# Optimization experiments

Hardware: AMD Instinct MI355X
Metric: run time of the kernel (lower is better)

The kernel has to match this reference:

```python
import jax, jax.numpy as jnp
import numpy as np

B, S, D = 32, 4096, 512

def setup_inputs() -> dict:
    key = jax.random.key(0)
    ks = jax.random.split(key, 5)
    scale = 1.0 / np.sqrt(D)
    return {
        "query": jax.random.normal(ks[0], (B, D), jnp.float32),
        "values": jax.random.normal(ks[1], (B, S, D), jnp.float32),
        "W1": jax.random.normal(ks[2], (D, D), jnp.float32) * scale,
        "b1": jnp.zeros((D,), jnp.float32),
        "W2": jax.random.normal(ks[3], (D, D), jnp.float32) * scale,
        "b2": jnp.zeros((D,), jnp.float32),
        "V": jax.random.normal(ks[4], (D, 1), jnp.float32) * scale,
        "bv": jnp.zeros((1,), jnp.float32),
    }

def reference(query, values, W1, b1, W2, b2, V, bv):
    # query: [B, D], values: [B, S, D]
    q_proj = query @ W1 + b1                      # [B, D]
    v_proj = jnp.einsum('bsd,de->bse', values, W2) + b2  # [B, S, D]
    hidden = jnp.tanh(q_proj[:, None, :] + v_proj)       # [B, S, D]
    score = jnp.einsum('bsd,de->bse', hidden, V) + bv    # [B, S, 1]
    attn = jax.nn.softmax(score, axis=1)                 # softmax over seq axis
    context = jnp.sum(attn * values, axis=1)             # [B, D]
    return (context, attn)
```

## Files before the change

kernel.cpp:

```cpp
#include <hip/hip_runtime.h>
#include <hip/hip_bf16.h>
#include <stdint.h>

#define NB 32
#define NS 4096
#define ND 512

typedef __attribute__((ext_vector_type(8))) short short8;
typedef __attribute__((ext_vector_type(4))) float floatx4;
typedef __attribute__((ext_vector_type(4))) unsigned int uint4v;

__device__ __forceinline__ short f2bf(float f) {
    unsigned int u = __builtin_bit_cast(unsigned int, f);
    return (short)((u + 0x8000u) >> 16);
}

__device__ __forceinline__ unsigned int cvt_pk_bf16(float lo, float hi) {
    unsigned int r;
    asm("v_cvt_pk_bf16_f32 %0, %1, %2" : "=v"(r) : "v"(lo), "v"(hi));
    return r;
}

__device__ __forceinline__ float fast_tanh(float x) {
    float e = __expf(2.0f * x);
    return 1.0f - 2.0f * __builtin_amdgcn_rcpf(e + 1.0f);
}

__global__ void __launch_bounds__(256) qproj_kernel(
    const float* __restrict__ query, const float* __restrict__ W1,
    const float* __restrict__ b1, const float* __restrict__ b2,
    float* __restrict__ qb) {
    const int b  = blockIdx.x;
    const int es = blockIdx.y;
    const int t  = threadIdx.x;
    const int col = t & 63, kc = t >> 6;
    __shared__ float q[ND];
    __shared__ float red[256];
    q[t] = query[b * ND + t];
    q[t + 256] = query[b * ND + t + 256];
    __syncthreads();
    float acc = 0.f;
    const float* wp = W1 + (size_t)(kc * 128) * ND + es * 64 + col;
    const float* qp = q + kc * 128;
#pragma unroll 8
    for (int k = 0; k < 128; k++)
        acc += qp[k] * wp[(size_t)k * ND];
    red[t] = acc;
    __syncthreads();
    if (t < 64) {
        float s = red[t] + red[t + 64] + red[t + 128] + red[t + 192];
        int e = es * 64 + t;
        qb[b * ND + e] = s + b1[e] + b2[e];
    }
}

__global__ void __launch_bounds__(256) w2t_kernel(
    const float* __restrict__ W2, unsigned short* __restrict__ W2Tt) {
    int g = blockIdx.x * 256 + threadIdx.x;
    int nt = g >> 14;
    int ks = (g >> 10) & 15;
    int kq = (g >> 8) & 3;
    int n  = g & 255;
    int e  = nt * 256 + n;
    int k0 = ks * 32 + kq * 8;
    short8 v;
#pragma unroll
    for (int j = 0; j < 8; j++)
        v[j] = f2bf(W2[(size_t)(k0 + j) * ND + e]);
    *(short8*)&W2Tt[(size_t)g * 8] = v;
}

__global__ void __launch_bounds__(256, 2) scores_kernel(
    const float* __restrict__ values, const unsigned short* __restrict__ W2Tt,
    const float* __restrict__ qb, const float* __restrict__ V,
    float* __restrict__ pscores) {
    const int st = blockIdx.x;
    const int b  = blockIdx.y;
    const int s0 = st * 64;

    __shared__ __align__(16) unsigned short sA[16][2048];
    __shared__ float sQb[ND];
    __shared__ float sV[ND];
    __shared__ float sRed[4][64];

    const int tid  = threadIdx.x;
    const int lane = tid & 63;
    const int wave = tid >> 6;
    const int mr = lane & 15;
    const int q  = lane >> 4;

    sQb[tid] = qb[b * ND + tid];
    sQb[tid + 256] = qb[b * ND + tid + 256];
    sV[tid]  = V[tid];
    sV[tid + 256] = V[tid + 256];

    const int arow = tid >> 2;
    const int ac   = tid & 3;
    const int ardo = arow * 32 + ((ac ^ ((tid >> 3) & 3)) * 8);
    const float* ag = values + ((size_t)b * NS + s0 + arow) * ND + ac * 8;

    {
        float4 aq[4][2];
#pragma unroll
        for (int u = 0; u < 4; u++) {
            aq[u][0] = *(const float4*)(ag + u * 32);
            aq[u][1] = *(const float4*)(ag + u * 32 + 4);
        }
#pragma unroll
        for (int ks = 0; ks < 16; ks++) {
            const float4 a0 = aq[ks & 3][0], a1 = aq[ks & 3][1];
            if (ks < 12) {
                aq[ks & 3][0] = *(const float4*)(ag + (ks + 4) * 32);
                aq[ks & 3][1] = *(const float4*)(ag + (ks + 4) * 32 + 4);
            }
            uint4v w;
            w.x = cvt_pk_bf16(a0.x, a0.y); w.y = cvt_pk_bf16(a0.z, a0.w);
            w.z = cvt_pk_bf16(a1.x, a1.y); w.w = cvt_pk_bf16(a1.z, a1.w);
            *(uint4v*)&sA[ks][ardo] = w;
        }
    }
    __syncthreads();

    const int afo = (q ^ ((mr >> 1) & 3)) * 8;
    const unsigned short* bp = W2Tt + (q * 256 + wave * 64 + mr) * 8;

    floatx4 acc[4][4] = {};
    float p[4][4] = {};
    short8 af[2][4], bq[2][4];

#pragma unroll
    for (int i = 0; i < 4; i++)
        af[0][i] = *(const short8*)&sA[0][(i * 16 + mr) * 32 + afo];
#pragma unroll
    for (int j = 0; j < 4; j++)
        bq[0][j] = *(const short8*)(bp + j * 128);

#pragma unroll
    for (int hk = 0; hk < 32; hk++) {
        const int cur = hk & 1, nxt = cur ^ 1;
        const int ks = hk & 15;

        if (hk < 31) {
            const unsigned short* bsrc = bp + (size_t)(hk + 1) * 8192;
#pragma unroll
            for (int j = 0; j < 4; j++)
                bq[nxt][j] = *(const short8*)(bsrc + j * 128);
#pragma unroll
            for (int i = 0; i < 4; i++)
                af[nxt][i] = *(const short8*)&sA[(hk + 1) & 15][(i * 16 + mr) * 32 + afo];
        }

        __builtin_amdgcn_s_setprio(1);
#pragma unroll
        for (int i = 0; i < 4; i++)
#pragma unroll
            for (int j = 0; j < 4; j++)
                acc[i][j] = __builtin_amdgcn_mfma_f32_16x16x32_bf16(af[cur][i], bq[cur][j], acc[i][j], 0, 0, 0);
        __builtin_amdgcn_s_setprio(0);

        if (ks == 15) {
            const int h = hk >> 4;
            float vcoef[4], qadd[4];
#pragma unroll
            for (int j = 0; j < 4; j++) {
                int col = h * 256 + wave * 64 + j * 16 + mr;
                vcoef[j] = sV[col];
                qadd[j]  = sQb[col];
            }
#pragma unroll
            for (int i = 0; i < 4; i++)
#pragma unroll
                for (int r = 0; r < 4; r++) {
                    float s = 0.f;
#pragma unroll
                    for (int j = 0; j < 4; j++)
                        s += fast_tanh(acc[i][j][r] + qadd[j]) * vcoef[j];
                    p[i][r] += s;
                    if (hk < 31) acc[i][0][r] = 0.f;
                }
            if (hk < 31) {
#pragma unroll
                for (int i = 0; i < 4; i++)
#pragma unroll
                    for (int j = 1; j < 4; j++)
                        acc[i][j] = floatx4{0.f, 0.f, 0.f, 0.f};
            }
        }
    }

#pragma unroll
    for (int i = 0; i < 4; i++) {
#pragma unroll
        for (int r = 0; r < 4; r++) {
            float v = p[i][r];
            v += __shfl_xor(v, 1);
            v += __shfl_xor(v, 2);
            v += __shfl_xor(v, 4);
            v += __shfl_xor(v, 8);
            if (mr == 0) sRed[wave][i * 16 + q * 4 + r] = v;
        }
    }
    __syncthreads();
    if (tid < 64) {
        float s = sRed[0][tid] + sRed[1][tid] + sRed[2][tid] + sRed[3][tid];
        pscores[(size_t)b * NS + s0 + tid] = s;
    }
}

__global__ void __launch_bounds__(256) softmax_kernel(
    const float* __restrict__ pscores, float* __restrict__ attn) {
    int b = blockIdx.x;
    int t = threadIdx.x;
    __shared__ float red[4];
    __shared__ float bcast[2];
    const float* sc = pscores + (size_t)b * NS;
    float v[16];
    float m = -1e30f;
#pragma unroll
    for (int i = 0; i < 16; i++) { v[i] = sc[t + i * 256]; m = fmaxf(m, v[i]); }
    for (int o = 32; o; o >>= 1) m = fmaxf(m, __shfl_xor(m, o));
    if ((t & 63) == 0) red[t >> 6] = m;
    __syncthreads();
    if (t == 0) bcast[0] = fmaxf(fmaxf(red[0], red[1]), fmaxf(red[2], red[3]));
    __syncthreads();
    m = bcast[0];
    float sum = 0.f;
#pragma unroll
    for (int i = 0; i < 16; i++) { v[i] = __expf(v[i] - m); sum += v[i]; }
    for (int o = 32; o; o >>= 1) sum += __shfl_xor(sum, o);
    if ((t & 63) == 0) red[t >> 6] = sum;
    __syncthreads();
    if (t == 0) bcast[1] = red[0] + red[1] + red[2] + red[3];
    __syncthreads();
    float inv = 1.0f / bcast[1];
    float* ao = attn + (size_t)b * NS;
#pragma unroll
    for (int i = 0; i < 16; i++) ao[t + i * 256] = v[i] * inv;
}

__global__ void __launch_bounds__(256) context_partial_kernel(
    const float* __restrict__ values, const float* __restrict__ attn,
    float* __restrict__ pctx) {
    int sc = blockIdx.x;
    int b  = blockIdx.y;
    int t  = threadIdx.x;
    __shared__ float sAttn[128];
    if (t < 128) sAttn[t] = attn[(size_t)b * NS + sc * 128 + t];
    __syncthreads();
    int d = t * 2;
    const float2* vp = (const float2*)(values + ((size_t)b * NS + sc * 128) * ND + d);
    float ax = 0.f, ay = 0.f;
#pragma unroll 8
    for (int s = 0; s < 128; s++) {
        float a = sAttn[s];
        float2 v = vp[(size_t)s * 256];
        ax += a * v.x; ay += a * v.y;
    }
    pctx[((size_t)sc * 32 + b) * ND + d]     = ax;
    pctx[((size_t)sc * 32 + b) * ND + d + 1] = ay;
}

__global__ void __launch_bounds__(256) context_reduce_kernel(
    const float* __restrict__ pctx, float* __restrict__ ctx) {
    int i = blockIdx.x * 256 + threadIdx.x;
    float s = 0.f;
#pragma unroll
    for (int p = 0; p < 32; p++) s += pctx[(size_t)p * (32 * ND) + i];
    ctx[i] = s;
}

extern "C" void kernel_launch(void* const* d_in, const int* in_sizes, int n_in,
                              void* d_out, int out_size, void* d_ws, size_t ws_size,
                              hipStream_t stream) {
    const float* query  = (const float*)d_in[0];
    const float* values = (const float*)d_in[1];
    const float* W1     = (const float*)d_in[2];
    const float* b1     = (const float*)d_in[3];
    const float* W2     = (const float*)d_in[4];
    const float* b2     = (const float*)d_in[5];
    const float* V      = (const float*)d_in[6];

    float* ctx_out  = (float*)d_out;
    float* attn_out = (float*)d_out + NB * ND;

    char* ws = (char*)d_ws;
    float*          qb      = (float*)ws;
    unsigned short* W2Tt    = (unsigned short*)(ws + (64 << 10));
    float*          pscores = (float*)(ws + (576 << 10));
    float*          pctx    = (float*)(ws + (1088 << 10));

    qproj_kernel<<<dim3(NB, 8), 256, 0, stream>>>(query, W1, b1, b2, qb);
    w2t_kernel<<<128, 256, 0, stream>>>(W2, W2Tt);
    scores_kernel<<<dim3(64, 32), 256, 0, stream>>>(values, W2Tt, qb, V, pscores);
    softmax_kernel<<<NB, 256, 0, stream>>>(pscores, attn_out);
    context_partial_kernel<<<dim3(32, 32), 256, 0, stream>>>(values, attn_out, pctx);
    context_reduce_kernel<<<64, 256, 0, stream>>>(pctx, ctx_out);
}
```

Baseline: 477.2 us.

## Fuse prep and softmax kernels, deepen B prefetch, use nontemporal value loads

Merges the q-projection and W2 transpose into one launch, and folds the softmax into the context-partial kernel so each block recomputes the row max and sum itself. The softmax_kernel launch and the attn read-back go away, at the cost of 32x redundant softmax reductions. In the scores kernel the W2 fragment prefetch is deepened to a 3-stage ring, which adds register pressure. The loads of values now use nontemporal hints to limit cache pollution.

New measurement: 459.9 us. 3.6% less time.

```diff
diff --git a/kernel.cpp b/kernel.cpp
--- a/kernel.cpp
+++ b/kernel.cpp
@@ -8,6 +8,7 @@
 
 typedef __attribute__((ext_vector_type(8))) short short8;
 typedef __attribute__((ext_vector_type(4))) float floatx4;
+typedef __attribute__((ext_vector_type(2))) float floatx2;
 typedef __attribute__((ext_vector_type(4))) unsigned int uint4v;
 
 __device__ __forceinline__ short f2bf(float f) {
@@ -26,48 +27,49 @@
     return 1.0f - 2.0f * __builtin_amdgcn_rcpf(e + 1.0f);
 }
 
-__global__ void __launch_bounds__(256) qproj_kernel(
+__global__ void __launch_bounds__(256) prep_kernel(
     const float* __restrict__ query, const float* __restrict__ W1,
     const float* __restrict__ b1, const float* __restrict__ b2,
-    float* __restrict__ qb) {
-    const int b  = blockIdx.x;
-    const int es = blockIdx.y;
+    const float* __restrict__ W2,
+    float* __restrict__ qb, unsigned short* __restrict__ W2Tt) {
+    const int bx = blockIdx.x;
     const int t  = threadIdx.x;
-    const int col = t & 63, kc = t >> 6;
-    __shared__ float q[ND];
-    __shared__ float red[256];
-    q[t] = query[b * ND + t];
-    q[t + 256] = query[b * ND + t + 256];
-    __syncthreads();
-    float acc = 0.f;
-    const float* wp = W1 + (size_t)(kc * 128) * ND + es * 64 + col;
-    const float* qp = q + kc * 128;
+    if (bx < 256) {
+        const int b  = bx >> 3;
+        const int es = bx & 7;
+        const int col = t & 63, kc = t >> 6;
+        __shared__ float q[ND];
+        __shared__ float red[256];
+        q[t] = query[b * ND + t];
+        q[t + 256] = query[b * ND + t + 256];
+        __syncthreads();
+        float acc = 0.f;
+        const float* wp = W1 + (size_t)(kc * 128) * ND + es * 64 + col;
+        const float* qp = q + kc * 128;
 #pragma unroll 8
-    for (int k = 0; k < 128; k++)
-        acc += qp[k] * wp[(size_t)k * ND];
-    red[t] = acc;
-    __syncthreads();
-    if (t < 64) {
-        float s = red[t] + red[t + 64] + red[t + 128] + red[t + 192];
-        int e = es * 64 + t;
-        qb[b * ND + e] = s + b1[e] + b2[e];
-    }
-}
-
-__global__ void __launch_bounds__(256) w2t_kernel(
-    const float* __restrict__ W2, unsigned short* __restrict__ W2Tt) {
-    int g = blockIdx.x * 256 + threadIdx.x;
-    int nt = g >> 14;
-    int ks = (g >> 10) & 15;
-    int kq = (g >> 8) & 3;
-    int n  = g & 255;
-    int e  = nt * 256 + n;
-    int k0 = ks * 32 + kq * 8;
-    short8 v;
-#pragma unroll
-    for (int j = 0; j < 8; j++)
-        v[j] = f2bf(W2[(size_t)(k0 + j) * ND + e]);
-    *(short8*)&W2Tt[(size_t)g * 8] = v;
+        for (int k = 0; k < 128; k++)
+            acc += qp[k] * wp[(size_t)k * ND];
+        red[t] = acc;
+        __syncthreads();
+        if (t < 64) {
+            float s = red[t] + red[t + 64] + red[t + 128] + red[t + 192];
+            int e = es * 64 + t;
+            qb[b * ND + e] = s + b1[e] + b2[e];
+        }
+    } else {
+        int g = (bx - 256) * 256 + t;
+        int nt = g >> 14;
+        int ks = (g >> 10) & 15;
+        int kq = (g >> 8) & 3;
+        int n  = g & 255;
+        int e  = nt * 256 + n;
+        int k0 = ks * 32 + kq * 8;
+        short8 v;
+#pragma unroll
+        for (int j = 0; j < 8; j++)
+            v[j] = f2bf(W2[(size_t)(k0 + j) * ND + e]);
+        *(short8*)&W2Tt[(size_t)g * 8] = v;
+    }
 }
 
 __global__ void __launch_bounds__(256, 2) scores_kernel(
@@ -100,18 +102,18 @@
     const float* ag = values + ((size_t)b * NS + s0 + arow) * ND + ac * 8;
 
     {
-        float4 aq[4][2];
+        floatx4 aq[4][2];
 #pragma unroll
         for (int u = 0; u < 4; u++) {
-            aq[u][0] = *(const float4*)(ag + u * 32);
-            aq[u][1] = *(const float4*)(ag + u * 32 + 4);
+            aq[u][0] = __builtin_nontemporal_load((const floatx4*)(ag + u * 32));
+            aq[u][1] = __builtin_nontemporal_load((const floatx4*)(ag + u * 32 + 4));
         }
 #pragma unroll
         for (int ks = 0; ks < 16; ks++) {
-            const float4 a0 = aq[ks & 3][0], a1 = aq[ks & 3][1];
+            const floatx4 a0 = aq[ks & 3][0], a1 = aq[ks & 3][1];
             if (ks < 12) {
-                aq[ks & 3][0] = *(const float4*)(ag + (ks + 4) * 32);
-                aq[ks & 3][1] = *(const float4*)(ag + (ks + 4) * 32 + 4);
+                aq[ks & 3][0] = __builtin_nontemporal_load((const floatx4*)(ag + (ks + 4) * 32));
+                aq[ks & 3][1] = __builtin_nontemporal_load((const floatx4*)(ag + (ks + 4) * 32 + 4));
             }
             uint4v w;
             w.x = cvt_pk_bf16(a0.x, a0.y); w.y = cvt_pk_bf16(a0.z, a0.w);
@@ -126,7 +128,7 @@
 
     floatx4 acc[4][4] = {};
     float p[4][4] = {};
-    short8 af[2][4], bq[2][4];
+    short8 af[2][4], bq[3][4];
 
 #pragma unroll
     for (int i = 0; i < 4; i++)
@@ -134,17 +136,22 @@
 #pragma unroll
     for (int j = 0; j < 4; j++)
         bq[0][j] = *(const short8*)(bp + j * 128);
+#pragma unroll
+    for (int j = 0; j < 4; j++)
+        bq[1][j] = *(const short8*)(bp + 8192 + j * 128);
 
 #pragma unroll
     for (int hk = 0; hk < 32; hk++) {
         const int cur = hk & 1, nxt = cur ^ 1;
         const int ks = hk & 15;
 
+        if (hk < 30) {
+            const unsigned short* bsrc = bp + (size_t)(hk + 2) * 8192;
+#pragma unroll
+            for (int j = 0; j < 4; j++)
+                bq[(hk + 2) % 3][j] = *(const short8*)(bsrc + j * 128);
+        }
         if (hk < 31) {
-            const unsigned short* bsrc = bp + (size_t)(hk + 1) * 8192;
-#pragma unroll
-            for (int j = 0; j < 4; j++)
-                bq[nxt][j] = *(const short8*)(bsrc + j * 128);
 #pragma unroll
             for (int i = 0; i < 4; i++)
                 af[nxt][i] = *(const short8*)&sA[(hk + 1) & 15][(i * 16 + mr) * 32 + afo];
@@ -155,7 +162,7 @@
         for (int i = 0; i < 4; i++)
 #pragma unroll
             for (int j = 0; j < 4; j++)
-                acc[i][j] = __builtin_amdgcn_mfma_f32_16x16x32_bf16(af[cur][i], bq[cur][j], acc[i][j], 0, 0, 0);
+                acc[i][j] = __builtin_amdgcn_mfma_f32_16x16x32_bf16(af[cur][i], bq[hk % 3][j], acc[i][j], 0, 0, 0);
         __builtin_amdgcn_s_setprio(0);
 
         if (ks == 15) {
@@ -207,54 +214,49 @@
     }
 }
 
-__global__ void __launch_bounds__(256) softmax_kernel(
-    const float* __restrict__ pscores, float* __restrict__ attn) {
-    int b = blockIdx.x;
-    int t = threadIdx.x;
-    __shared__ float red[4];
-    __shared__ float bcast[2];
-    const float* sc = pscores + (size_t)b * NS;
-    float v[16];
-    float m = -1e30f;
-#pragma unroll
-    for (int i = 0; i < 16; i++) { v[i] = sc[t + i * 256]; m = fmaxf(m, v[i]); }
-    for (int o = 32; o; o >>= 1) m = fmaxf(m, __shfl_xor(m, o));
-    if ((t & 63) == 0) red[t >> 6] = m;
-    __syncthreads();
-    if (t == 0) bcast[0] = fmaxf(fmaxf(red[0], red[1]), fmaxf(red[2], red[3]));
-    __syncthreads();
-    m = bcast[0];
-    float sum = 0.f;
-#pragma unroll
-    for (int i = 0; i < 16; i++) { v[i] = __expf(v[i] - m); sum += v[i]; }
-    for (int o = 32; o; o >>= 1) sum += __shfl_xor(sum, o);
-    if ((t & 63) == 0) red[t >> 6] = sum;
-    __syncthreads();
-    if (t == 0) bcast[1] = red[0] + red[1] + red[2] + red[3];
-    __syncthreads();
-    float inv = 1.0f / bcast[1];
-    float* ao = attn + (size_t)b * NS;
-#pragma unroll
-    for (int i = 0; i < 16; i++) ao[t + i * 256] = v[i] * inv;
-}
-
-__global__ void __launch_bounds__(256) context_partial_kernel(
-    const float* __restrict__ values, const float* __restrict__ attn,
-    float* __restrict__ pctx) {
+__global__ void __launch_bounds__(256) context_softmax_kernel(
+    const float* __restrict__ values, const float* __restrict__ pscores,
+    float* __restrict__ attn, float* __restrict__ pctx) {
     int sc = blockIdx.x;
     int b  = blockIdx.y;
     int t  = threadIdx.x;
     __shared__ float sAttn[128];
-    if (t < 128) sAttn[t] = attn[(size_t)b * NS + sc * 128 + t];
+    __shared__ float red[4];
+    __shared__ float bcast[2];
+    const float* srow = pscores + (size_t)b * NS;
+    float v[16];
+    float m = -1e30f;
+#pragma unroll
+    for (int i = 0; i < 16; i++) { v[i] = srow[t + i * 256]; m = fmaxf(m, v[i]); }
+    for (int o = 32; o; o >>= 1) m = fmaxf(m, __shfl_xor(m, o));
+    if ((t & 63) == 0) red[t >> 6] = m;
+    __syncthreads();
+    if (t == 0) bcast[0] = fmaxf(fmaxf(red[0], red[1]), fmaxf(red[2], red[3]));
+    __syncthreads();
+    m = bcast[0];
+    float sum = 0.f;
+#pragma unroll
+    for (int i = 0; i < 16; i++) sum += __expf(v[i] - m);
+    for (int o = 32; o; o >>= 1) sum += __shfl_xor(sum, o);
+    if ((t & 63) == 0) red[t >> 6] = sum;
+    __syncthreads();
+    if (t == 0) bcast[1] = red[0] + red[1] + red[2] + red[3];
+    __syncthreads();
+    float inv = 1.0f / bcast[1];
+    if (t < 128) {
+        float w = __expf(srow[sc * 128 + t] - m) * inv;
+        attn[(size_t)b * NS + sc * 128 + t] = w;
+        sAttn[t] = w;
+    }
     __syncthreads();
     int d = t * 2;
-    const float2* vp = (const float2*)(values + ((size_t)b * NS + sc * 128) * ND + d);
+    const float* vp = values + ((size_t)b * NS + sc * 128) * ND + d;
     float ax = 0.f, ay = 0.f;
 #pragma unroll 8
     for (int s = 0; s < 128; s++) {
         float a = sAttn[s];
-        float2 v = vp[(size_t)s * 256];
-        ax += a * v.x; ay += a * v.y;
+        floatx2 vv = __builtin_nontemporal_load((const floatx2*)(vp + (size_t)s * ND));
+        ax += a * vv.x; ay += a * vv.y;
     }
     pctx[((size_t)sc * 32 + b) * ND + d]     = ax;
     pctx[((size_t)sc * 32 + b) * ND + d + 1] = ay;
@@ -289,10 +291,8 @@
     float*          pscores = (float*)(ws + (576 << 10));
     float*          pctx    = (float*)(ws + (1088 << 10));
 
-    qproj_kernel<<<dim3(NB, 8), 256, 0, stream>>>(query, W1, b1, b2, qb);
-    w2t_kernel<<<128, 256, 0, stream>>>(W2, W2Tt);
+    prep_kernel<<<384, 256, 0, stream>>>(query, W1, b1, b2, W2, qb, W2Tt);
     scores_kernel<<<dim3(64, 32), 256, 0, stream>>>(values, W2Tt, qb, V, pscores);
-    softmax_kernel<<<NB, 256, 0, stream>>>(pscores, attn_out);
-    context_partial_kernel<<<dim3(32, 32), 256, 0, stream>>>(values, attn_out, pctx);
+    context_softmax_kernel<<<dim3(32, 32), 256, 0, stream>>>(values, pscores, attn_out, pctx);
     context_reduce_kernel<<<64, 256, 0, stream>>>(pctx, ctx_out);
 }
```
